# Kernel optimization log

Hardware: AMD Instinct MI355X
Metric: run time of the kernel (lower is better)

The kernel has to match this reference:

```python
import jax, jax.numpy as jnp
import numpy as np

N, E, D, H, G = 50000, 800000, 256, 256, 64
EPS = 1e-5

def setup_inputs() -> dict:
    key = jax.random.key(0)
    ks = jax.random.split(key, 16)
    s_in = float(np.sqrt(2.0 / D))   # He fan_in init
    s_h = float(np.sqrt(2.0 / H))
    inp = {}
    inp['x'] = jax.random.normal(ks[0], (N, D), jnp.float32)
    inp['edge_index'] = jax.random.randint(ks[1], (2, E), 0, N)
    inp['batch'] = jnp.sort(jax.random.randint(ks[2], (N,), 0, G))
    inp['bn_in_g'] = jnp.ones((D,), jnp.float32)
    inp['bn_in_b'] = jnp.zeros((D,), jnp.float32)
    for i in range(3):
        fan = D if i == 0 else H
        inp[f'W{i}'] = jax.random.normal(ks[3 + i], (fan, H), jnp.float32) * float(np.sqrt(2.0 / fan))
        inp[f'b{i}'] = jnp.zeros((H,), jnp.float32)
        inp[f'bn{i}_g'] = jnp.ones((H,), jnp.float32)
        inp[f'bn{i}_b'] = jnp.zeros((H,), jnp.float32)
    inp['Wa1'] = jax.random.normal(ks[6], (H, H // 2), jnp.float32) * s_h
    inp['ba1'] = jnp.zeros((H // 2,), jnp.float32)
    inp['Wa2'] = jax.random.normal(ks[7], (H // 2, 1), jnp.float32) * float(np.sqrt(2.0 / (H // 2)))
    inp['ba2'] = jnp.zeros((1,), jnp.float32)
    inp['Wo'] = jax.random.normal(ks[8], (H, 2), jnp.float32) * s_h
    inp['bo'] = jnp.zeros((2,), jnp.float32)
    return inp


def _bn(x, g, b):
    # BatchNorm1d, batch statistics (training-mode normalization), biased var
    m = jnp.mean(x, axis=0)
    v = jnp.mean(jnp.square(x - m), axis=0)
    return (x - m) * jax.lax.rsqrt(v + EPS) * g + b


def _gcn(x, src, dst, W, b):
    h = x @ W  # [N, H]
    n = x.shape[0]
    deg = jax.ops.segment_sum(jnp.ones_like(src, x.dtype), dst, num_segments=n) + 1.0  # +1 self-loop
    dinv = jax.lax.rsqrt(deg)  # [N]
    msg = h[src] * (dinv[src] * dinv[dst])[:, None]          # gather + edgewise scale
    agg = jax.ops.segment_sum(msg, dst, num_segments=n)      # scatter-add at dst
    return agg + h * (dinv * dinv)[:, None] + b               # self-loop term fused


def reference(x, edge_index, batch, bn_in_g, bn_in_b,
              W0, b0, bn0_g, bn0_b, W1, b1, bn1_g, bn1_b, W2, b2, bn2_g, bn2_b,
              Wa1, ba1, Wa2, ba2, Wo, bo):
    src, dst = edge_index[0], edge_index[1]
    x = _bn(x, bn_in_g, bn_in_b)  # dropout = identity (eval)
    # layer 0
    xp = _bn(jax.nn.relu(_gcn(x, src, dst, W0, b0)), bn0_g, bn0_b)
    # layers 1..2 with residual
    for (W, b, g, bb) in ((W1, b1, bn1_g, bn1_b), (W2, b2, bn2_g, bn2_b)):
        xn = _bn(jax.nn.relu(_gcn(xp, src, dst, W, b)), g, bb)
        xp = xn + xp
    # attention over all nodes (softmax along node dim, as in source)
    scores = jax.nn.leaky_relu(xp @ Wa1 + ba1, 0.01) @ Wa2 + ba2  # [N,1]
    w = jax.nn.softmax(scores, axis=0)
    xw = xp * w
    cnt = jax.ops.segment_sum(jnp.ones((xp.shape[0],), xp.dtype), batch, num_segments=G)
    pooled = jax.ops.segment_sum(xw, batch, num_segments=G) / jnp.maximum(cnt, 1.0)[:, None]
    return pooled @ Wo + bo  # [G, 2]
```

## Files before the change

### kernel.cpp

```cpp
#include <hip/hip_runtime.h>

#define N_NODES 50000
#define N_EDGES 800000
#define DIM 256
#define NG 64
#define EPS_BN 1e-5f
#define NB_AGG 3125
#define NB_COL 512
#define NSPLIT 32

typedef _Float16 f16;
typedef _Float16 half8 __attribute__((ext_vector_type(8)));
typedef _Float16 half4 __attribute__((ext_vector_type(4)));
typedef float floatx4 __attribute__((ext_vector_type(4)));

__device__ __forceinline__ int fkey(float f) { int i = __float_as_int(f); return (i >= 0) ? i : (i ^ 0x7fffffff); }
__device__ __forceinline__ float keyf(int k) { return __int_as_float((k >= 0) ? k : (k ^ 0x7fffffff)); }

__global__ __launch_bounds__(256) void col_stats_kernel(const float* __restrict__ X, int n,
                                                        float* __restrict__ part) {
    int c = threadIdx.x;
    float s = 0.f, q = 0.f;
    for (int i = blockIdx.x; i < n; i += gridDim.x) {
        float v = X[(size_t)i * DIM + c];
        s += v; q += v * v;
    }
    part[(size_t)blockIdx.x * 512 + c] = s;
    part[(size_t)blockIdx.x * 512 + DIM + c] = q;
}

__global__ __launch_bounds__(256) void reduce_finalize_kernel(const float* __restrict__ part, int nrows,
                                                              float* __restrict__ p2, int* __restrict__ counter,
                                                              const float* __restrict__ g, const float* __restrict__ b,
                                                              float* __restrict__ affine, float inv_n) {
    int col = blockIdx.x * 256 + threadIdx.x;
    int chunk = (nrows + NSPLIT - 1) / NSPLIT;
    int r0 = blockIdx.y * chunk;
    int r1 = min(r0 + chunk, nrows);
    float t = 0.f;
    for (int r = r0; r < r1; r++) t += part[(size_t)r * 512 + col];
    p2[(size_t)blockIdx.y * 512 + col] = t;
    __threadfence();
    __shared__ int lastf;
    if (threadIdx.x == 0) lastf = (atomicAdd(counter, 1) == 2 * NSPLIT - 1) ? 1 : 0;
    __syncthreads();
    if (lastf) {
        __threadfence();
        int c = threadIdx.x;
        float s = 0.f, q = 0.f;
#pragma unroll
        for (int r = 0; r < NSPLIT; r++) {
            s += p2[(size_t)r * 512 + c];
            q += p2[(size_t)r * 512 + DIM + c];
        }
        float m = s * inv_n;
        float v = q * inv_n - m * m;
        float rstd = rsqrtf(v + EPS_BN);
        float A = rstd * g[c];
        affine[c] = A;
        affine[DIM + c] = b[c] - m * A;
    }
}

__global__ void convert_all_kernel(const float* __restrict__ W0, const float* __restrict__ W1,
                                   const float* __restrict__ W2, const float* __restrict__ Wa1,
                                   f16* __restrict__ T0, f16* __restrict__ T1,
                                   f16* __restrict__ T2, f16* __restrict__ T3) {
    int idx = blockIdx.x * 256 + threadIdx.x;
    if (idx < 196608) {
        int w = idx >> 16, r = idx & 65535;
        const float* W = (w == 0) ? W0 : (w == 1) ? W1 : W2;
        f16* T = (w == 0) ? T0 : (w == 1) ? T1 : T2;
        int m = r >> 8, k = r & 255;
        T[r] = (f16)W[(size_t)k * 256 + m];
    } else {
        int r = idx - 196608;
        int m = r >> 8, k = r & 255;
        T3[r] = (f16)Wa1[(size_t)k * 128 + m];
    }
}

__global__ void count_bounds_kernel(const int* __restrict__ dst, int ne, int* __restrict__ cnt,
                                    int* __restrict__ lpos,
                                    const int* __restrict__ batch, int n, int* __restrict__ start) {
    int gb = blockIdx.x;
    if (gb < NB_AGG) {
        for (int i = gb * 256 + threadIdx.x; i < ne; i += NB_AGG * 256)
            lpos[i] = atomicAdd(&cnt[dst[i]], 1);
    } else {
        int i = (gb - NB_AGG) * 256 + threadIdx.x;
        if (i < n) {
            int b = batch[i];
            if (i == 0 || batch[i - 1] != b) start[b] = i;
        }
    }
}

#define SCHUNK 2048
__global__ __launch_bounds__(256) void scan1_kernel(const int* __restrict__ cnt, int n,
                                                    int* __restrict__ outp, int* __restrict__ bsums,
                                                    float* __restrict__ dinv) {
    __shared__ int lds[256];
    int t = threadIdx.x;
    int base = blockIdx.x * SCHUNK + t * 8;
    int v[8]; int s = 0;
#pragma unroll
    for (int j = 0; j < 8; j++) {
        int id = base + j;
        int x = 0;
        if (id < n) { x = cnt[id]; dinv[id] = rsqrtf((float)x + 1.0f); }
        v[j] = s; s += x;
    }
    lds[t] = s; __syncthreads();
    for (int o = 1; o < 256; o <<= 1) {
        int add = (t >= o) ? lds[t - o] : 0;
        __syncthreads();
        lds[t] += add;
        __syncthreads();
    }
    int excl = lds[t] - s;
#pragma unroll
    for (int j = 0; j < 8; j++) { int id = base + j; if (id < n) outp[id] = excl + v[j]; }
    if (t == 255) bsums[blockIdx.x] = lds[255];
}

__global__ void scan3_kernel(int* __restrict__ outp, const int* __restrict__ bsums, int n, int total) {
    int i = blockIdx.x * blockDim.x + threadIdx.x;
    if (i < n) {
        int k = i / SCHUNK;
        int pref = 0;
        for (int j = 0; j < k; j++) pref += bsums[j];
        outp[i] += pref;
    }
    if (i == 0) outp[n] = total;
}

__global__ void scatter_kernel(const int* __restrict__ src, const int* __restrict__ dst,
                               const int* __restrict__ lpos, int ne,
                               const int* __restrict__ rowp, int* __restrict__ ss) {
    for (int e = blockIdx.x * blockDim.x + threadIdx.x; e < ne; e += gridDim.x * blockDim.x)
        ss[rowp[dst[e]] + lpos[e]] = src[e];
}

__global__ void graph_offsets2_kernel(const int* __restrict__ start, int* __restrict__ off, int* __restrict__ cnt,
                                      int* __restrict__ maxkey) {
    if (threadIdx.x == 0 && blockIdx.x == 0) {
        int nxt = N_NODES;
        for (int g = NG - 1; g >= 0; --g) {
            int s = start[g];
            int o = (s < 0) ? nxt : s;
            off[g] = o;
            cnt[g] = nxt - o;
            nxt = o;
        }
        maxkey[0] = 0x80000000;
    }
}

__global__ __launch_bounds__(256) void gcn_agg_kernel(const f16* __restrict__ h, const int* __restrict__ rowp,
                                                      const int* __restrict__ ss, const float* __restrict__ dinv,
                                                      const float* __restrict__ bias, f16* __restrict__ out,
                                                      float* __restrict__ part, int n) {
    int wave = threadIdx.x >> 6;
    int lane = threadIdx.x & 63;
    int c = lane * 4;
    float4 bv = *(const float4*)&bias[c];
    float s0a = 0.f, s1a = 0.f, s2a = 0.f, s3a = 0.f;
    float q0a = 0.f, q1a = 0.f, q2a = 0.f, q3a = 0.f;
    for (int row = blockIdx.x * 4 + wave; row < n; row += gridDim.x * 4) {
        float ax = 0.f, ay = 0.f, az = 0.f, aw = 0.f;
        int e0 = rowp[row], e1 = rowp[row + 1];
        int e = e0;
        for (; e + 3 < e1; e += 4) {
            int i0 = ss[e], i1 = ss[e + 1], i2 = ss[e + 2], i3 = ss[e + 3];
            half4 h0 = *(const half4*)&h[((size_t)i0 << 8) + c];
            half4 h1 = *(const half4*)&h[((size_t)i1 << 8) + c];
            half4 h2 = *(const half4*)&h[((size_t)i2 << 8) + c];
            half4 h3 = *(const half4*)&h[((size_t)i3 << 8) + c];
            ax += ((float)h0[0] + (float)h1[0]) + ((float)h2[0] + (float)h3[0]);
            ay += ((float)h0[1] + (float)h1[1]) + ((float)h2[1] + (float)h3[1]);
            az += ((float)h0[2] + (float)h1[2]) + ((float)h2[2] + (float)h3[2]);
            aw += ((float)h0[3] + (float)h1[3]) + ((float)h2[3] + (float)h3[3]);
        }
        for (; e < e1; e++) {
            int si = ss[e];
            half4 hv = *(const half4*)&h[((size_t)si << 8) + c];
            ax += (float)hv[0]; ay += (float)hv[1]; az += (float)hv[2]; aw += (float)hv[3];
        }
        float di = dinv[row];
        half4 hs = *(const half4*)&h[((size_t)row << 8) + c];
        float rx = di * (ax + (float)hs[0]) + bv.x;
        float ry = di * (ay + (float)hs[1]) + bv.y;
        float rz = di * (az + (float)hs[2]) + bv.z;
        float rw = di * (aw + (float)hs[3]) + bv.w;
        half4 o; o[0] = (f16)rx; o[1] = (f16)ry; o[2] = (f16)rz; o[3] = (f16)rw;
        *(half4*)&out[((size_t)row << 8) + c] = o;
        float t;
        t = fmaxf(rx, 0.f); s0a += t; q0a += t * t;
        t = fmaxf(ry, 0.f); s1a += t; q1a += t * t;
        t = fmaxf(rz, 0.f); s2a += t; q2a += t * t;
        t = fmaxf(rw, 0.f); s3a += t; q3a += t * t;
    }
    __shared__ float sred[4][64][4];
    __shared__ float qred[4][64][4];
    sred[wave][lane][0] = s0a; sred[wave][lane][1] = s1a; sred[wave][lane][2] = s2a; sred[wave][lane][3] = s3a;
    qred[wave][lane][0] = q0a; qred[wave][lane][1] = q1a; qred[wave][lane][2] = q2a; qred[wave][lane][3] = q3a;
    __syncthreads();
    if (wave == 0) {
        size_t base = (size_t)blockIdx.x * 512;
        float4 a = make_float4(0.f, 0.f, 0.f, 0.f), qv = make_float4(0.f, 0.f, 0.f, 0.f);
#pragma unroll
        for (int ww = 0; ww < 4; ww++) {
            a.x += sred[ww][lane][0]; a.y += sred[ww][lane][1]; a.z += sred[ww][lane][2]; a.w += sred[ww][lane][3];
            qv.x += qred[ww][lane][0]; qv.y += qred[ww][lane][1]; qv.z += qred[ww][lane][2]; qv.w += qred[ww][lane][3];
        }
        *(float4*)&part[base + c] = a;
        *(float4*)&part[base + DIM + c] = qv;
    }
}

#define BM 128
#define BN 128
#define BK 32
#define LDP 40
__global__ __launch_bounds__(256) void gemm_fused_kernel(const float* __restrict__ Xf32, const f16* __restrict__ Ch,
                                                         const f16* __restrict__ Aold, f16* __restrict__ Afout,
                                                         const float* __restrict__ affine,
                                                         const f16* __restrict__ Wt, f16* __restrict__ Cout,
                                                         const float* __restrict__ scale, int n, int K, int M) {
    __shared__ __align__(16) f16 As[BM * LDP];
    __shared__ __align__(16) f16 Bs[BN * LDP];
    __shared__ float sA[256], sB[256];
    int tid = threadIdx.x;
    if (tid < 256) { sA[tid] = affine[tid]; sB[tid] = affine[256 + tid]; }
    int wave = tid >> 6, lane = tid & 63;
    int wm = wave >> 1, wn = wave & 1;
    int q = lane >> 4, l16 = lane & 15;
    int bm = blockIdx.x * BM, bn = blockIdx.y * BN;
    int kc = (tid & 3) * 8;
    int writer = (Afout != nullptr) && (blockIdx.y == 0);
    floatx4 acc[4][4] = {};
    __syncthreads();
    for (int k0 = 0; k0 < K; k0 += BK) {
        float a8[8], b8[8];
#pragma unroll
        for (int j = 0; j < 8; j++) { a8[j] = sA[k0 + kc + j]; b8[j] = sB[k0 + kc + j]; }
#pragma unroll
        for (int rr = 0; rr < 2; rr++) {
            int cidx = tid + rr * 256;
            int row = cidx >> 2;
            int arow = bm + row; if (arow >= n) arow = n - 1;
            float v[8];
            if (Xf32) {
                float4 x0 = *(const float4*)&Xf32[(size_t)arow * K + k0 + kc];
                float4 x1 = *(const float4*)&Xf32[(size_t)arow * K + k0 + kc + 4];
                v[0] = x0.x; v[1] = x0.y; v[2] = x0.z; v[3] = x0.w;
                v[4] = x1.x; v[5] = x1.y; v[6] = x1.z; v[7] = x1.w;
            } else {
                half8 ch = *(const half8*)&Ch[(size_t)arow * K + k0 + kc];
#pragma unroll
                for (int j = 0; j < 8; j++) v[j] = fmaxf((float)ch[j], 0.f);
            }
            half8 af;
            if (Aold) {
                half8 ao = *(const half8*)&Aold[(size_t)arow * K + k0 + kc];
#pragma unroll
                for (int j = 0; j < 8; j++) af[j] = (f16)(v[j] * a8[j] + b8[j] + (float)ao[j]);
            } else {
#pragma unroll
                for (int j = 0; j < 8; j++) af[j] = (f16)(v[j] * a8[j] + b8[j]);
            }
            *(float4*)&As[row * LDP + kc] = *(float4*)&af;
            if (writer && bm + row < n) *(half8*)&Afout[(size_t)arow * K + k0 + kc] = af;
            int brow = bn + row;
            *(float4*)&Bs[row * LDP + kc] = *(const float4*)&Wt[(size_t)brow * K + k0 + kc];
        }
        __syncthreads();
        half8 afr[4], bfr[4];
#pragma unroll
        for (int i = 0; i < 4; i++) afr[i] = *(half8*)&As[(wm * 64 + i * 16 + l16) * LDP + q * 8];
#pragma unroll
        for (int j = 0; j < 4; j++) bfr[j] = *(half8*)&Bs[(wn * 64 + j * 16 + l16) * LDP + q * 8];
#pragma unroll
        for (int i = 0; i < 4; i++)
#pragma unroll
            for (int j = 0; j < 4; j++)
                acc[i][j] = __builtin_amdgcn_mfma_f32_16x16x32_f16(afr[i], bfr[j], acc[i][j], 0, 0, 0);
        __syncthreads();
    }
#pragma unroll
    for (int i = 0; i < 4; i++) {
#pragma unroll
        for (int r = 0; r < 4; r++) {
            int row = bm + wm * 64 + i * 16 + q * 4 + r;
            if (row < n) {
                float sc = scale[row];
#pragma unroll
                for (int j = 0; j < 4; j++) {
                    int col = bn + wn * 64 + j * 16 + l16;
                    Cout[(size_t)row * M + col] = (f16)(acc[i][j][r] * sc);
                }
            }
        }
    }
}

__global__ __launch_bounds__(256) void gemm_attn_kernel(const f16* __restrict__ Ch, const f16* __restrict__ Aold,
                                                        f16* __restrict__ Afout, const float* __restrict__ affine,
                                                        const f16* __restrict__ Wt,
                                                        const float* __restrict__ ba1, const float* __restrict__ Wa2,
                                                        const float* __restrict__ ba2, float* __restrict__ score,
                                                        int* __restrict__ maxkey, int n, int K) {
    __shared__ __align__(16) f16 As[BM * LDP];
    __shared__ __align__(16) f16 Bs[128 * LDP];
    __shared__ float sA[256], sB[256];
    __shared__ float scred[128][2];
    int tid = threadIdx.x;
    if (tid < 256) { sA[tid] = affine[tid]; sB[tid] = affine[256 + tid]; }
    int wave = tid >> 6, lane = tid & 63;
    int wm = wave >> 1, wn = wave & 1;
    int q = lane >> 4, l16 = lane & 15;
    int bm = blockIdx.x * BM;
    int kc = (tid & 3) * 8;
    floatx4 acc[4][4] = {};
    __syncthreads();
    for (int k0 = 0; k0 < K; k0 += BK) {
        float a8[8], b8[8];
#pragma unroll
        for (int j = 0; j < 8; j++) { a8[j] = sA[k0 + kc + j]; b8[j] = sB[k0 + kc + j]; }
#pragma unroll
        for (int rr = 0; rr < 2; rr++) {
            int cidx = tid + rr * 256;
            int row = cidx >> 2;
            int arow = bm + row; if (arow >= n) arow = n - 1;
            half8 ch = *(const half8*)&Ch[(size_t)arow * K + k0 + kc];
            half8 ao = *(const half8*)&Aold[(size_t)arow * K + k0 + kc];
            half8 af;
#pragma unroll
            for (int j = 0; j < 8; j++)
                af[j] = (f16)(fmaxf((float)ch[j], 0.f) * a8[j] + b8[j] + (float)ao[j]);
            *(float4*)&As[row * LDP + kc] = *(float4*)&af;
            if (bm + row < n) *(half8*)&Afout[(size_t)arow * K + k0 + kc] = af;
            *(float4*)&Bs[row * LDP + kc] = *(const float4*)&Wt[(size_t)row * K + k0 + kc];
        }
        __syncthreads();
        half8 afr[4], bfr[4];
#pragma unroll
        for (int i = 0; i < 4; i++) afr[i] = *(half8*)&As[(wm * 64 + i * 16 + l16) * LDP + q * 8];
#pragma unroll
        for (int j = 0; j < 4; j++) bfr[j] = *(half8*)&Bs[(wn * 64 + j * 16 + l16) * LDP + q * 8];
#pragma unroll
        for (int i = 0; i < 4; i++)
#pragma unroll
            for (int j = 0; j < 4; j++)
                acc[i][j] = __builtin_amdgcn_mfma_f32_16x16x32_f16(afr[i], bfr[j], acc[i][j], 0, 0, 0);
        __syncthreads();
    }
    float ba1v[4], wa2v[4];
#pragma unroll
    for (int j = 0; j < 4; j++) {
        int col = wn * 64 + j * 16 + l16;
        ba1v[j] = ba1[col];
        wa2v[j] = Wa2[col];
    }
#pragma unroll
    for (int i = 0; i < 4; i++)
#pragma unroll
        for (int r = 0; r < 4; r++) {
            float p = 0.f;
#pragma unroll
            for (int j = 0; j < 4; j++) {
                float v = acc[i][j][r] + ba1v[j];
                v = (v > 0.f) ? v : 0.01f * v;
                p += v * wa2v[j];
            }
#pragma unroll
            for (int o = 1; o < 16; o <<= 1) p += __shfl_xor(p, o);
            if (l16 == 0) scred[wm * 64 + i * 16 + q * 4 + r][wn] = p;
        }
    __syncthreads();
    __shared__ float mred[128];
    if (tid < 128) {
        int grow = bm + tid;
        float sc = scred[tid][0] + scred[tid][1] + ba2[0];
        if (grow < n) score[grow] = sc; else sc = -3.0e38f;
        mred[tid] = sc;
    }
    __syncthreads();
    for (int o = 64; o > 0; o >>= 1) {
        if (tid < o && tid + o < 128) mred[tid] = fmaxf(mred[tid], mred[tid + o]);
        __syncthreads();
    }
    if (tid == 0) atomicMax(maxkey, fkey(mred[0]));
}

__global__ __launch_bounds__(256) void pool_kernel(const f16* __restrict__ Af, const float* __restrict__ score,
                                                   const int* __restrict__ offs, const int* __restrict__ cnts,
                                                   const int* __restrict__ maxkey, float* __restrict__ expsum,
                                                   float* __restrict__ pooled) {
    float mx = keyf(maxkey[0]);
    int c = threadIdx.x;
    int g = blockIdx.x;
    int st = offs[g], cn = cnts[g];
    float acc = 0.f, esum = 0.f;
    for (int i = (int)blockIdx.y; i < cn; i += 32) {
        int i1 = i + 8, i2 = i + 16, i3 = i + 24;
        float s0 = score[st + i];
        float s1 = (i1 < cn) ? score[st + i1] : -3.0e38f;
        float s2 = (i2 < cn) ? score[st + i2] : -3.0e38f;
        float s3 = (i3 < cn) ? score[st + i3] : -3.0e38f;
        float e0 = expf(s0 - mx), e1 = expf(s1 - mx), e2 = expf(s2 - mx), e3 = expf(s3 - mx);
        float a0 = (float)Af[(size_t)(st + i) * DIM + c];
        float a1 = (i1 < cn) ? (float)Af[(size_t)(st + i1) * DIM + c] : 0.f;
        float a2 = (i2 < cn) ? (float)Af[(size_t)(st + i2) * DIM + c] : 0.f;
        float a3 = (i3 < cn) ? (float)Af[(size_t)(st + i3) * DIM + c] : 0.f;
        acc += a0 * e0 + a1 * e1 + a2 * e2 + a3 * e3;
        esum += (e0 + e1) + (e2 + e3);
    }
    atomicAdd(&pooled[g * DIM + c], acc);
    if (c == 0) atomicAdd(expsum, esum);
}

__global__ __launch_bounds__(256) void out_kernel(const float* __restrict__ pooled, const int* __restrict__ cnt,
                                                  const float* __restrict__ expsum, const float* __restrict__ Wo,
                                                  const float* __restrict__ bo, float* __restrict__ out) {
    __shared__ float l0[256], l1[256];
    int g = blockIdx.x, c = threadIdx.x;
    float scale = 1.f / (expsum[0] * fmaxf((float)cnt[g], 1.f));
    float v = pooled[g * DIM + c] * scale;
    l0[c] = v * Wo[c * 2];
    l1[c] = v * Wo[c * 2 + 1];
    __syncthreads();
    for (int o = 128; o > 0; o >>= 1) {
        if (c < o) { l0[c] += l0[c + o]; l1[c] += l1[c + o]; }
        __syncthreads();
    }
    if (c == 0) { out[g * 2] = l0[0] + bo[0]; out[g * 2 + 1] = l1[0] + bo[1]; }
}

extern "C" void kernel_launch(void* const* d_in, const int* in_sizes, int n_in,
                              void* d_out, int out_size, void* d_ws, size_t ws_size,
                              hipStream_t stream) {
    const float* x       = (const float*)d_in[0];
    const int*   ei      = (const int*)d_in[1];
    const int*   batch   = (const int*)d_in[2];
    const float* bn_in_g = (const float*)d_in[3];
    const float* bn_in_b = (const float*)d_in[4];
    const float* Ws[3]   = {(const float*)d_in[5],  (const float*)d_in[9],  (const float*)d_in[13]};
    const float* bs[3]   = {(const float*)d_in[6],  (const float*)d_in[10], (const float*)d_in[14]};
    const float* gs[3]   = {(const float*)d_in[7],  (const float*)d_in[11], (const float*)d_in[15]};
    const float* bbs[3]  = {(const float*)d_in[8],  (const float*)d_in[12], (const float*)d_in[16]};
    const float* Wa1 = (const float*)d_in[17];
    const float* ba1 = (const float*)d_in[18];
    const float* Wa2 = (const float*)d_in[19];
    const float* ba2 = (const float*)d_in[20];
    const float* Wo  = (const float*)d_in[21];
    const float* bo  = (const float*)d_in[22];

    char* w = (char*)d_ws;
    size_t off = 0;
    auto alloc = [&](size_t bytes) -> void* {
        void* p = w + off;
        off += (bytes + 255) & ~(size_t)255;
        return p;
    };
    int*   deg     = (int*)alloc((size_t)N_NODES * 4);
    float* pooled  = (float*)alloc((size_t)NG * DIM * 4);
    int*   counters = (int*)alloc(4 * 4);
    float* expsum  = (float*)alloc(4);
    size_t zero_span = off;
    float* stats_part = (float*)alloc((size_t)NB_AGG * 512 * 4);
    float* stats_p2   = (float*)alloc((size_t)NSPLIT * 512 * 4);
    float* affine  = (float*)alloc(512 * 4);
    f16*   AfA  = (f16*)alloc((size_t)N_NODES * DIM * 2);
    f16*   AfB  = (f16*)alloc((size_t)N_NODES * DIM * 2);
    f16*   Bh   = (f16*)alloc((size_t)N_NODES * DIM * 2);
    f16*   Chb  = (f16*)alloc((size_t)N_NODES * DIM * 2);
    f16*   Wt[3];
    for (int l = 0; l < 3; l++) Wt[l] = (f16*)alloc((size_t)DIM * DIM * 2);
    f16*   Wa1t = (f16*)alloc((size_t)128 * DIM * 2);
    int* sorted_src = (int*)alloc((size_t)N_EDGES * 4);
    int* lpos   = (int*)alloc((size_t)N_EDGES * 4);
    float* dinv = (float*)alloc((size_t)N_NODES * 4);
    int* rowp   = (int*)alloc((size_t)(N_NODES + 1) * 4);
    float* score = (float*)alloc((size_t)N_NODES * 4);
    int* bsums   = (int*)alloc(64 * 4);
    int* maxkey  = (int*)alloc(16);
    int* gstart  = (int*)alloc(64 * 4);
    int* cnt_g   = (int*)alloc(64 * 4);
    int* off_g   = (int*)alloc(64 * 4);

    const int* src = ei;
    const int* dst = ei + N_EDGES;
    const int NSCAN = (N_NODES + SCHUNK - 1) / SCHUNK;
    const float inv_n = 1.f / N_NODES;

    hipMemsetAsync(d_ws, 0, zero_span, stream);
    hipMemsetAsync(gstart, 0xff, 64 * 4, stream);

    count_bounds_kernel<<<NB_AGG + 196, 256, 0, stream>>>(dst, N_EDGES, deg, lpos, batch, N_NODES, gstart);
    scan1_kernel<<<NSCAN, 256, 0, stream>>>(deg, N_NODES, rowp, bsums, dinv);
    scan3_kernel<<<(N_NODES + 255) / 256, 256, 0, stream>>>(rowp, bsums, N_NODES, N_EDGES);
    scatter_kernel<<<NB_AGG, 256, 0, stream>>>(src, dst, lpos, N_EDGES, rowp, sorted_src);
    graph_offsets2_kernel<<<1, 64, 0, stream>>>(gstart, off_g, cnt_g, maxkey);

    convert_all_kernel<<<896, 256, 0, stream>>>(Ws[0], Ws[1], Ws[2], Wa1, Wt[0], Wt[1], Wt[2], Wa1t);

    col_stats_kernel<<<NB_COL, 256, 0, stream>>>(x, N_NODES, stats_part);
    reduce_finalize_kernel<<<dim3(2, NSPLIT), 256, 0, stream>>>(stats_part, NB_COL, stats_p2, counters + 0,
                                                                bn_in_g, bn_in_b, affine, inv_n);

    dim3 ggrid((N_NODES + BM - 1) / BM, DIM / BN);
    gemm_fused_kernel<<<ggrid, 256, 0, stream>>>(x, nullptr, nullptr, nullptr, affine, Wt[0], Bh, dinv, N_NODES, DIM, DIM);
    gcn_agg_kernel<<<NB_AGG, 256, 0, stream>>>(Bh, rowp, sorted_src, dinv, bs[0], Chb, stats_part, N_NODES);
    reduce_finalize_kernel<<<dim3(2, NSPLIT), 256, 0, stream>>>(stats_part, NB_AGG, stats_p2, counters + 1,
                                                                gs[0], bbs[0], affine, inv_n);
    gemm_fused_kernel<<<ggrid, 256, 0, stream>>>(nullptr, Chb, nullptr, AfA, affine, Wt[1], Bh, dinv, N_NODES, DIM, DIM);
    gcn_agg_kernel<<<NB_AGG, 256, 0, stream>>>(Bh, rowp, sorted_src, dinv, bs[1], Chb, stats_part, N_NODES);
    reduce_finalize_kernel<<<dim3(2, NSPLIT), 256, 0, stream>>>(stats_part, NB_AGG, stats_p2, counters + 2,
                                                                gs[1], bbs[1], affine, inv_n);
    gemm_fused_kernel<<<ggrid, 256, 0, stream>>>(nullptr, Chb, AfA, AfB, affine, Wt[2], Bh, dinv, N_NODES, DIM, DIM);
    gcn_agg_kernel<<<NB_AGG, 256, 0, stream>>>(Bh, rowp, sorted_src, dinv, bs[2], Chb, stats_part, N_NODES);
    reduce_finalize_kernel<<<dim3(2, NSPLIT), 256, 0, stream>>>(stats_part, NB_AGG, stats_p2, counters + 3,
                                                                gs[2], bbs[2], affine, inv_n);

    gemm_attn_kernel<<<(N_NODES + BM - 1) / BM, 256, 0, stream>>>(Chb, AfB, AfA, affine, Wa1t,
                                                                  ba1, Wa2, ba2, score, maxkey, N_NODES, DIM);

    pool_kernel<<<dim3(NG, 8), 256, 0, stream>>>(AfA, score, off_g, cnt_g, maxkey, expsum, pooled);
    out_kernel<<<NG, 256, 0, stream>>>(pooled, cnt_g, expsum, Wo, bo, (float*)d_out);
}
```

Measured before the change: 702.5 us.

## Fuse preprocessing kernels, use chained single-pass scan, widen GEMM tile to full N

Merges the degree count, graph-boundary, weight-conversion and input column-stats kernels into one prep launch. The two-pass scan becomes a single-pass decoupled chained scan, and the group-offset computation moves into an extra block of the scatter kernel. The GEMM now computes all 256 output columns per block, which drops the second grid dimension and the redundant A-tile loads and normalization. The intent is fewer launches and less repeated A traffic, at the cost of more registers per thread in the GEMM and a spin-wait between scan blocks.

```diff
diff --git a/kernel.cpp b/kernel.cpp
--- a/kernel.cpp
+++ b/kernel.cpp
@@ -8,6 +8,11 @@
 #define NB_AGG 3125
 #define NB_COL 512
 #define NSPLIT 32
+#define PB_CNT 3125
+#define PB_BND 196
+#define PB_CVT 896
+#define PB_CST 512
+#define PB_TOTAL (PB_CNT + PB_BND + PB_CVT + PB_CST)
 
 typedef _Float16 f16;
 typedef _Float16 half8 __attribute__((ext_vector_type(8)));
@@ -17,16 +22,49 @@
 __device__ __forceinline__ int fkey(float f) { int i = __float_as_int(f); return (i >= 0) ? i : (i ^ 0x7fffffff); }
 __device__ __forceinline__ float keyf(int k) { return __int_as_float((k >= 0) ? k : (k ^ 0x7fffffff)); }
 
-__global__ __launch_bounds__(256) void col_stats_kernel(const float* __restrict__ X, int n,
-                                                        float* __restrict__ part) {
-    int c = threadIdx.x;
-    float s = 0.f, q = 0.f;
-    for (int i = blockIdx.x; i < n; i += gridDim.x) {
-        float v = X[(size_t)i * DIM + c];
-        s += v; q += v * v;
-    }
-    part[(size_t)blockIdx.x * 512 + c] = s;
-    part[(size_t)blockIdx.x * 512 + DIM + c] = q;
+__global__ __launch_bounds__(256) void prep_kernel(const int* __restrict__ dst, int* __restrict__ cnt,
+                                                   int* __restrict__ lpos,
+                                                   const int* __restrict__ batch, int* __restrict__ start,
+                                                   const float* __restrict__ W0, const float* __restrict__ W1,
+                                                   const float* __restrict__ W2, const float* __restrict__ Wa1,
+                                                   f16* __restrict__ T0, f16* __restrict__ T1,
+                                                   f16* __restrict__ T2, f16* __restrict__ T3,
+                                                   const float* __restrict__ X, float* __restrict__ part) {
+    int gb = blockIdx.x;
+    int tid = threadIdx.x;
+    if (gb < PB_CNT) {
+        for (int i = gb * 256 + tid; i < N_EDGES; i += PB_CNT * 256)
+            lpos[i] = atomicAdd(&cnt[dst[i]], 1);
+    } else if (gb < PB_CNT + PB_BND) {
+        int i = (gb - PB_CNT) * 256 + tid;
+        if (i < N_NODES) {
+            int b = batch[i];
+            if (i == 0 || batch[i - 1] != b) start[b] = i + 1;
+        }
+    } else if (gb < PB_CNT + PB_BND + PB_CVT) {
+        int idx = (gb - PB_CNT - PB_BND) * 256 + tid;
+        if (idx < 196608) {
+            int w = idx >> 16, r = idx & 65535;
+            const float* W = (w == 0) ? W0 : (w == 1) ? W1 : W2;
+            f16* T = (w == 0) ? T0 : (w == 1) ? T1 : T2;
+            int m = r >> 8, k = r & 255;
+            T[r] = (f16)W[(size_t)k * 256 + m];
+        } else {
+            int r = idx - 196608;
+            int m = r >> 8, k = r & 255;
+            T3[r] = (f16)Wa1[(size_t)k * 128 + m];
+        }
+    } else {
+        int blk = gb - (PB_CNT + PB_BND + PB_CVT);
+        int c = tid;
+        float s = 0.f, q = 0.f;
+        for (int i = blk; i < N_NODES; i += PB_CST) {
+            float v = X[(size_t)i * DIM + c];
+            s += v; q += v * v;
+        }
+        part[(size_t)blk * 512 + c] = s;
+        part[(size_t)blk * 512 + DIM + c] = q;
+    }
 }
 
 __global__ __launch_bounds__(256) void reduce_finalize_kernel(const float* __restrict__ part, int nrows,
@@ -62,47 +100,15 @@
     }
 }
 
-__global__ void convert_all_kernel(const float* __restrict__ W0, const float* __restrict__ W1,
-                                   const float* __restrict__ W2, const float* __restrict__ Wa1,
-                                   f16* __restrict__ T0, f16* __restrict__ T1,
-                                   f16* __restrict__ T2, f16* __restrict__ T3) {
-    int idx = blockIdx.x * 256 + threadIdx.x;
-    if (idx < 196608) {
-        int w = idx >> 16, r = idx & 65535;
-        const float* W = (w == 0) ? W0 : (w == 1) ? W1 : W2;
-        f16* T = (w == 0) ? T0 : (w == 1) ? T1 : T2;
-        int m = r >> 8, k = r & 255;
-        T[r] = (f16)W[(size_t)k * 256 + m];
-    } else {
-        int r = idx - 196608;
-        int m = r >> 8, k = r & 255;
-        T3[r] = (f16)Wa1[(size_t)k * 128 + m];
-    }
-}
-
-__global__ void count_bounds_kernel(const int* __restrict__ dst, int ne, int* __restrict__ cnt,
-                                    int* __restrict__ lpos,
-                                    const int* __restrict__ batch, int n, int* __restrict__ start) {
-    int gb = blockIdx.x;
-    if (gb < NB_AGG) {
-        for (int i = gb * 256 + threadIdx.x; i < ne; i += NB_AGG * 256)
-            lpos[i] = atomicAdd(&cnt[dst[i]], 1);
-    } else {
-        int i = (gb - NB_AGG) * 256 + threadIdx.x;
-        if (i < n) {
-            int b = batch[i];
-            if (i == 0 || batch[i - 1] != b) start[b] = i;
-        }
-    }
-}
-
 #define SCHUNK 2048
-__global__ __launch_bounds__(256) void scan1_kernel(const int* __restrict__ cnt, int n,
-                                                    int* __restrict__ outp, int* __restrict__ bsums,
-                                                    float* __restrict__ dinv) {
+__global__ __launch_bounds__(256) void scan_kernel(const int* __restrict__ cnt, int n,
+                                                   int* __restrict__ outp, int* __restrict__ chain,
+                                                   float* __restrict__ dinv) {
     __shared__ int lds[256];
+    __shared__ int sprefix;
     int t = threadIdx.x;
-    int base = blockIdx.x * SCHUNK + t * 8;
+    int b = blockIdx.x;
+    int base = b * SCHUNK + t * 8;
     int v[8]; int s = 0;
 #pragma unroll
     for (int j = 0; j < 8; j++) {
@@ -119,42 +125,45 @@
         __syncthreads();
     }
     int excl = lds[t] - s;
-#pragma unroll
-    for (int j = 0; j < 8; j++) { int id = base + j; if (id < n) outp[id] = excl + v[j]; }
-    if (t == 255) bsums[blockIdx.x] = lds[255];
-}
-
-__global__ void scan3_kernel(int* __restrict__ outp, const int* __restrict__ bsums, int n, int total) {
-    int i = blockIdx.x * blockDim.x + threadIdx.x;
-    if (i < n) {
-        int k = i / SCHUNK;
+    int total = lds[255];
+    if (t == 0) {
         int pref = 0;
-        for (int j = 0; j < k; j++) pref += bsums[j];
-        outp[i] += pref;
-    }
-    if (i == 0) outp[n] = total;
-}
-
-__global__ void scatter_kernel(const int* __restrict__ src, const int* __restrict__ dst,
-                               const int* __restrict__ lpos, int ne,
-                               const int* __restrict__ rowp, int* __restrict__ ss) {
-    for (int e = blockIdx.x * blockDim.x + threadIdx.x; e < ne; e += gridDim.x * blockDim.x)
+        if (b > 0) {
+            int p;
+            do { p = atomicAdd(&chain[b - 1], 0); } while (p == 0);
+            pref = p - 1;
+        }
+        atomicExch(&chain[b], pref + total + 1);
+        sprefix = pref;
+    }
+    __syncthreads();
+    int pref = sprefix;
+#pragma unroll
+    for (int j = 0; j < 8; j++) { int id = base + j; if (id < n) outp[id] = pref + excl + v[j]; }
+    if (b == gridDim.x - 1 && t == 0) outp[n] = pref + total;
+}
+
+__global__ void scatter_offsets_kernel(const int* __restrict__ src, const int* __restrict__ dst,
+                                       const int* __restrict__ lpos, int ne,
+                                       const int* __restrict__ rowp, int* __restrict__ ss,
+                                       const int* __restrict__ start, int* __restrict__ off,
+                                       int* __restrict__ cnt, int* __restrict__ maxkey) {
+    if (blockIdx.x == NB_AGG) {
+        if (threadIdx.x == 0) {
+            int nxt = N_NODES;
+            for (int g = NG - 1; g >= 0; --g) {
+                int s = start[g];
+                int o = (s == 0) ? nxt : (s - 1);
+                off[g] = o;
+                cnt[g] = nxt - o;
+                nxt = o;
+            }
+            maxkey[0] = 0x80000000;
+        }
+        return;
+    }
+    for (int e = blockIdx.x * blockDim.x + threadIdx.x; e < ne; e += NB_AGG * 256)
         ss[rowp[dst[e]] + lpos[e]] = src[e];
-}
-
-__global__ void graph_offsets2_kernel(const int* __restrict__ start, int* __restrict__ off, int* __restrict__ cnt,
-                                      int* __restrict__ maxkey) {
-    if (threadIdx.x == 0 && blockIdx.x == 0) {
-        int nxt = N_NODES;
-        for (int g = NG - 1; g >= 0; --g) {
-            int s = start[g];
-            int o = (s < 0) ? nxt : s;
-            off[g] = o;
-            cnt[g] = nxt - o;
-            nxt = o;
-        }
-        maxkey[0] = 0x80000000;
-    }
 }
 
 __global__ __launch_bounds__(256) void gcn_agg_kernel(const f16* __restrict__ h, const int* __restrict__ rowp,
@@ -220,26 +229,25 @@
 }
 
 #define BM 128
-#define BN 128
 #define BK 32
 #define LDP 40
 __global__ __launch_bounds__(256) void gemm_fused_kernel(const float* __restrict__ Xf32, const f16* __restrict__ Ch,
                                                          const f16* __restrict__ Aold, f16* __restrict__ Afout,
                                                          const float* __restrict__ affine,
                                                          const f16* __restrict__ Wt, f16* __restrict__ Cout,
-                                                         const float* __restrict__ scale, int n, int K, int M) {
+                                                         const float* __restrict__ scale, int n, int K) {
     __shared__ __align__(16) f16 As[BM * LDP];
-    __shared__ __align__(16) f16 Bs[BN * LDP];
+    __shared__ __align__(16) f16 Bs[256 * LDP];
     __shared__ float sA[256], sB[256];
     int tid = threadIdx.x;
-    if (tid < 256) { sA[tid] = affine[tid]; sB[tid] = affine[256 + tid]; }
+    sA[tid] = affine[tid]; sB[tid] = affine[256 + tid];
     int wave = tid >> 6, lane = tid & 63;
     int wm = wave >> 1, wn = wave & 1;
     int q = lane >> 4, l16 = lane & 15;
-    int bm = blockIdx.x * BM, bn = blockIdx.y * BN;
+    int bm = blockIdx.x * BM;
     int kc = (tid & 3) * 8;
-    int writer = (Afout != nullptr) && (blockIdx.y == 0);
-    floatx4 acc[4][4] = {};
+    int writer = (Afout != nullptr);
+    floatx4 acc[4][8] = {};
     __syncthreads();
     for (int k0 = 0; k0 < K; k0 += BK) {
         float a8[8], b8[8];
@@ -272,19 +280,23 @@
             }
             *(float4*)&As[row * LDP + kc] = *(float4*)&af;
             if (writer && bm + row < n) *(half8*)&Afout[(size_t)arow * K + k0 + kc] = af;
-            int brow = bn + row;
-            *(float4*)&Bs[row * LDP + kc] = *(const float4*)&Wt[(size_t)brow * K + k0 + kc];
-        }
-        __syncthreads();
-        half8 afr[4], bfr[4];
+        }
+#pragma unroll
+        for (int rr = 0; rr < 4; rr++) {
+            int cidx = tid + rr * 256;
+            int row = cidx >> 2;
+            *(float4*)&Bs[row * LDP + kc] = *(const float4*)&Wt[(size_t)row * K + k0 + kc];
+        }
+        __syncthreads();
+        half8 afr[4], bfr[8];
 #pragma unroll
         for (int i = 0; i < 4; i++) afr[i] = *(half8*)&As[(wm * 64 + i * 16 + l16) * LDP + q * 8];
 #pragma unroll
-        for (int j = 0; j < 4; j++) bfr[j] = *(half8*)&Bs[(wn * 64 + j * 16 + l16) * LDP + q * 8];
+        for (int j = 0; j < 8; j++) bfr[j] = *(half8*)&Bs[(wn * 128 + j * 16 + l16) * LDP + q * 8];
 #pragma unroll
         for (int i = 0; i < 4; i++)
 #pragma unroll
-            for (int j = 0; j < 4; j++)
+            for (int j = 0; j < 8; j++)
                 acc[i][j] = __builtin_amdgcn_mfma_f32_16x16x32_f16(afr[i], bfr[j], acc[i][j], 0, 0, 0);
         __syncthreads();
     }
@@ -296,9 +308,9 @@
             if (row < n) {
                 float sc = scale[row];
 #pragma unroll
-                for (int j = 0; j < 4; j++) {
-                    int col = bn + wn * 64 + j * 16 + l16;
-                    Cout[(size_t)row * M + col] = (f16)(acc[i][j][r] * sc);
+                for (int j = 0; j < 8; j++) {
+                    int col = wn * 128 + j * 16 + l16;
+                    Cout[(size_t)row * 256 + col] = (f16)(acc[i][j][r] * sc);
                 }
             }
         }
@@ -316,7 +328,7 @@
     __shared__ float sA[256], sB[256];
     __shared__ float scred[128][2];
     int tid = threadIdx.x;
-    if (tid < 256) { sA[tid] = affine[tid]; sB[tid] = affine[256 + tid]; }
+    sA[tid] = affine[tid]; sB[tid] = affine[256 + tid];
     int wave = tid >> 6, lane = tid & 63;
     int wm = wave >> 1, wn = wave & 1;
     int q = lane >> 4, l16 = lane & 15;
@@ -465,6 +477,8 @@
         return p;
     };
     int*   deg     = (int*)alloc((size_t)N_NODES * 4);
+    int*   gstart  = (int*)alloc(64 * 4);
+    int*   chain   = (int*)alloc(32 * 4);
     float* pooled  = (float*)alloc((size_t)NG * DIM * 4);
     int*   counters = (int*)alloc(4 * 4);
     float* expsum  = (float*)alloc(4);
@@ -484,9 +498,7 @@
     float* dinv = (float*)alloc((size_t)N_NODES * 4);
     int* rowp   = (int*)alloc((size_t)(N_NODES + 1) * 4);
     float* score = (float*)alloc((size_t)N_NODES * 4);
-    int* bsums   = (int*)alloc(64 * 4);
     int* maxkey  = (int*)alloc(16);
-    int* gstart  = (int*)alloc(64 * 4);
     int* cnt_g   = (int*)alloc(64 * 4);
     int* off_g   = (int*)alloc(64 * 4);
 
@@ -496,36 +508,32 @@
     const float inv_n = 1.f / N_NODES;
 
     hipMemsetAsync(d_ws, 0, zero_span, stream);
-    hipMemsetAsync(gstart, 0xff, 64 * 4, stream);
-
-    count_bounds_kernel<<<NB_AGG + 196, 256, 0, stream>>>(dst, N_EDGES, deg, lpos, batch, N_NODES, gstart);
-    scan1_kernel<<<NSCAN, 256, 0, stream>>>(deg, N_NODES, rowp, bsums, dinv);
-    scan3_kernel<<<(N_NODES + 255) / 256, 256, 0, stream>>>(rowp, bsums, N_NODES, N_EDGES);
-    scatter_kernel<<<NB_AGG, 256, 0, stream>>>(src, dst, lpos, N_EDGES, rowp, sorted_src);
-    graph_offsets2_kernel<<<1, 64, 0, stream>>>(gstart, off_g, cnt_g, maxkey);
-
-    convert_all_kernel<<<896, 256, 0, stream>>>(Ws[0], Ws[1], Ws[2], Wa1, Wt[0], Wt[1], Wt[2], Wa1t);
-
-    col_stats_kernel<<<NB_COL, 256, 0, stream>>>(x, N_NODES, stats_part);
+
+    prep_kernel<<<PB_TOTAL, 256, 0, stream>>>(dst, deg, lpos, batch, gstart,
+                                              Ws[0], Ws[1], Ws[2], Wa1, Wt[0], Wt[1], Wt[2], Wa1t,
+                                              x, stats_part);
+    scan_kernel<<<NSCAN, 256, 0, stream>>>(deg, N_NODES, rowp, chain, dinv);
+    scatter_offsets_kernel<<<NB_AGG + 1, 256, 0, stream>>>(src, dst, lpos, N_EDGES, rowp, sorted_src,
+                                                           gstart, off_g, cnt_g, maxkey);
     reduce_finalize_kernel<<<dim3(2, NSPLIT), 256, 0, stream>>>(stats_part, NB_COL, stats_p2, counters + 0,
                                                                 bn_in_g, bn_in_b, affine, inv_n);
 
-    dim3 ggrid((N_NODES + BM - 1) / BM, DIM / BN);
-    gemm_fused_kernel<<<ggrid, 256, 0, stream>>>(x, nullptr, nullptr, nullptr, affine, Wt[0], Bh, dinv, N_NODES, DIM, DIM);
+    const int NGB = (N_NODES + BM - 1) / BM;
+    gemm_fused_kernel<<<NGB, 256, 0, stream>>>(x, nullptr, nullptr, nullptr, affine, Wt[0], Bh, dinv, N_NODES, DIM);
     gcn_agg_kernel<<<NB_AGG, 256, 0, stream>>>(Bh, rowp, sorted_src, dinv, bs[0], Chb, stats_part, N_NODES);
     reduce_finalize_kernel<<<dim3(2, NSPLIT), 256, 0, stream>>>(stats_part, NB_AGG, stats_p2, counters + 1,
                                                                 gs[0], bbs[0], affine, inv_n);
-    gemm_fused_kernel<<<ggrid, 256, 0, stream>>>(nullptr, Chb, nullptr, AfA, affine, Wt[1], Bh, dinv, N_NODES, DIM, DIM);
+    gemm_fused_kernel<<<NGB, 256, 0, stream>>>(nullptr, Chb, nullptr, AfA, affine, Wt[1], Bh, dinv, N_NODES, DIM);
     gcn_agg_kernel<<<NB_AGG, 256, 0, stream>>>(Bh, rowp, sorted_src, dinv, bs[1], Chb, stats_part, N_NODES);
     reduce_finalize_kernel<<<dim3(2, NSPLIT), 256, 0, stream>>>(stats_part, NB_AGG, stats_p2, counters + 2,
                                                                 gs[1], bbs[1], affine, inv_n);
-    gemm_fused_kernel<<<ggrid, 256, 0, stream>>>(nullptr, Chb, AfA, AfB, affine, Wt[2], Bh, dinv, N_NODES, DIM, DIM);
+    gemm_fused_kernel<<<NGB, 256, 0, stream>>>(nullptr, Chb, AfA, AfB, affine, Wt[2], Bh, dinv, N_NODES, DIM);
     gcn_agg_kernel<<<NB_AGG, 256, 0, stream>>>(Bh, rowp, sorted_src, dinv, bs[2], Chb, stats_part, N_NODES);
     reduce_finalize_kernel<<<dim3(2, NSPLIT), 256, 0, stream>>>(stats_part, NB_AGG, stats_p2, counters + 3,
                                                                 gs[2], bbs[2], affine, inv_n);
 
-    gemm_attn_kernel<<<(N_NODES + BM - 1) / BM, 256, 0, stream>>>(Chb, AfB, AfA, affine, Wa1t,
-                                                                  ba1, Wa2, ba2, score, maxkey, N_NODES, DIM);
+    gemm_attn_kernel<<<NGB, 256, 0, stream>>>(Chb, AfB, AfA, affine, Wa1t,
+                                              ba1, Wa2, ba2, score, maxkey, N_NODES, DIM);
 
     pool_kernel<<<dim3(NG, 8), 256, 0, stream>>>(AfA, score, off_g, cnt_g, maxkey, expsum, pooled);
     out_kernel<<<NG, 256, 0, stream>>>(pooled, cnt_g, expsum, Wo, bo, (float*)d_out);
```

After: 702.7 us. No clear change (+0.0%).
